# Performance work log

Measured on AMD Instinct MI355X. Metric: run time of the kernel, lower is better.

The kernel has to match this reference:

```python
import jax, jax.numpy as jnp
import numpy as np
from jax import lax

HARD_RANK = 5
HARD_PROB = 0.5
MARGIN = 0.0
EPS = 1e-6  # F.pairwise_distance default eps (added to the difference)


def setup_inputs() -> dict:
    key = jax.random.key(0)
    x = jax.random.normal(key, (8192, 2, 256), dtype=jnp.float32)
    return {"x": x}


def _l2norm(v):
    # torch F.normalize: v / max(||v||, 1e-12)
    n = jnp.sqrt(jnp.sum(v * v, axis=1, keepdims=True))
    return v / jnp.maximum(n, 1e-12)


def reference(x):
    B, _, D = x.shape
    a = _l2norm(x[:, 0, :])  # anchors, unit norm -> ||a_i||^2 = 1
    p = _l2norm(x[:, 1, :])  # positives, unit norm

    # Full anchor-vs-positive distance matrix via GEMM (no [B,B,D] tensor).
    # torch pairwise_distance uses ||a - p + eps||, expand exactly:
    # ||a-p+eps*1||^2 = ||a||^2 + ||p||^2 - 2 a.p + 2*eps*(sum(a)-sum(p)) + D*eps^2
    am = lax.stop_gradient(a)
    pm = lax.stop_gradient(p)
    ip = am @ pm.T                          # [B, B]
    ra = jnp.sum(am, axis=1)                # [B]
    rp = jnp.sum(pm, axis=1)                # [B]
    d2 = 2.0 - 2.0 * ip + 2.0 * EPS * (ra[:, None] - rp[None, :]) + D * EPS * EPS
    dist = jnp.sqrt(jnp.maximum(d2, 0.0))

    # Exclude self (excidx drops idx) by masking diagonal to +inf.
    dmine = jnp.where(jnp.eye(B, dtype=bool), jnp.inf, dist)

    # hard_rank smallest distances per row (rank 0 = hardest negative).
    _, top_idx = lax.top_k(-dmine, HARD_RANK)   # [B, HARD_RANK]

    # With prob hard_prob pick the hardest; else uniform among top hard_rank.
    kr = jax.random.key(1)
    k1, k2 = jax.random.split(kr)
    coin = jax.random.uniform(k1, (B,)) < HARD_PROB
    rand_rank = jax.random.randint(k2, (B,), 0, HARD_RANK)
    rank = jnp.where(coin, 0, rand_rank)
    negidx = top_idx[jnp.arange(B), rank]       # [B]

    neg = p[negidx, :]
    pos_d2 = jnp.sum(jnp.square(a - p + EPS), axis=1)
    neg_d2 = jnp.sum(jnp.square(a - neg + EPS), axis=1)
    return jnp.mean(jax.nn.relu(pos_d2 - neg_d2 + MARGIN))
```

## Files before the change

kernel.cpp:

```cpp
#include <hip/hip_runtime.h>
#include <hip/hip_bf16.h>
#include <stdint.h>


#define NB 8192
#define NCG 32
#define EPSF 1e-6f

typedef int i32x4 __attribute__((ext_vector_type(4)));

struct U2 { uint32_t x, y; };

__host__ __device__ __forceinline__ uint32_t rotl32(uint32_t v, int n) {
  return (v << n) | (v >> (32 - n));
}

__host__ __device__ __forceinline__ U2 tf2x32(uint32_t k0, uint32_t k1,
                                              uint32_t x0, uint32_t x1) {
  uint32_t k2 = k0 ^ k1 ^ 0x1BD11BDAu;
#define TF_R(r) { x0 += x1; x1 = rotl32(x1, r); x1 ^= x0; }
  x0 += k0; x1 += k1;
  TF_R(13) TF_R(15) TF_R(26) TF_R(6)
  x0 += k1; x1 += k2 + 1u;
  TF_R(17) TF_R(29) TF_R(16) TF_R(24)
  x0 += k2; x1 += k0 + 2u;
  TF_R(13) TF_R(15) TF_R(26) TF_R(6)
  x0 += k0; x1 += k1 + 3u;
  TF_R(17) TF_R(29) TF_R(16) TF_R(24)
  x0 += k1; x1 += k2 + 4u;
  TF_R(13) TF_R(15) TF_R(26) TF_R(6)
  x0 += k2; x1 += k0 + 5u;
#undef TF_R
  U2 r; r.x = x0; r.y = x1; return r;
}

__device__ __forceinline__ uint32_t rng_word(U2 r) { return r.x ^ r.y; }

#define FINS5(T0, T1, T2, T3, T4, C) {            \
    const float _t0 = T0, _t1 = T1, _t2 = T2, _t3 = T3, _t4 = T4, _c = C; \
    T0 = fmaxf(_t0, _c);                          \
    T1 = __builtin_amdgcn_fmed3f(_c, _t0, _t1);   \
    T2 = __builtin_amdgcn_fmed3f(_c, _t1, _t2);   \
    T3 = __builtin_amdgcn_fmed3f(_c, _t2, _t3);   \
    T4 = __builtin_amdgcn_fmed3f(_c, _t3, _t4); }

__device__ __forceinline__ void gload16(const void* g, void* l) {
  __builtin_amdgcn_global_load_lds(
      (const __attribute__((address_space(1))) unsigned int*)g,
      (__attribute__((address_space(3))) unsigned int*)l, 16, 0, 0);
}

__global__ __launch_bounds__(256) void prep_kernel(
    const float* __restrict__ x,
    char* __restrict__ aq8, char* __restrict__ pq8) {
  const int w = threadIdx.x >> 6, l = threadIdx.x & 63;
  const int row = blockIdx.x * 4 + w;
  const float4* xr = (const float4*)(x + (size_t)row * 512);
  const float4 a4 = xr[l];
  const float4 p4 = xr[64 + l];
  float sa = a4.x * a4.x + a4.y * a4.y + a4.z * a4.z + a4.w * a4.w;
  float sp = p4.x * p4.x + p4.y * p4.y + p4.z * p4.z + p4.w * p4.w;
#pragma unroll
  for (int off = 32; off; off >>= 1) { sa += __shfl_xor(sa, off); sp += __shfl_xor(sp, off); }
  const float ia = 127.0f / fmaxf(sqrtf(sa), 1e-12f);
  const float ip_ = 127.0f / fmaxf(sqrtf(sp), 1e-12f);
  const int qa0 = (int)rintf(a4.x * ia), qa1 = (int)rintf(a4.y * ia);
  const int qa2 = (int)rintf(a4.z * ia), qa3 = (int)rintf(a4.w * ia);
  const int qp0 = (int)rintf(p4.x * ip_), qp1 = (int)rintf(p4.y * ip_);
  const int qp2 = (int)rintf(p4.z * ip_), qp3 = (int)rintf(p4.w * ip_);
  const uint32_t ua = (qa0 & 255) | ((qa1 & 255) << 8) |
                      ((qa2 & 255) << 16) | ((uint32_t)(qa3 & 255) << 24);
  const uint32_t up = (qp0 & 255) | ((qp1 & 255) << 8) |
                      ((qp2 & 255) << 16) | ((uint32_t)(qp3 & 255) << 24);
  *(uint32_t*)(aq8 + (size_t)row * 256 + l * 4) = ua;
  *(uint32_t*)(pq8 + (size_t)row * 256 + l * 4) = up;
}

__global__ __launch_bounds__(512, 2) void dist_topk_kernel(
    const char* __restrict__ aq8, const char* __restrict__ pq8,
    uint32_t* __restrict__ part) {
  __shared__ __align__(16) char smem[49152];

  const int tid = threadIdx.x;
  const int w = tid >> 6, l = tid & 63;
  const int lo = l & 15, hi = l >> 4;
  const int wr = w >> 2, wc = w & 3;

  const int b = blockIdx.x;
  const int xcd = b & 7, j = b >> 3;
  const int rb = (xcd >> 1) * 16 + (j >> 4);
  const int cb = (xcd & 1) * 16 + (j & 15);
  const int row0 = rb * 128, col0 = cb * 256;
  const bool hasDiag = (cb == (rb >> 1));

  i32x4 acc[4][4];
#pragma unroll
  for (int aq = 0; aq < 4; ++aq)
#pragma unroll
    for (int pq = 0; pq < 4; ++pq) { i32x4 z = {0, 0, 0, 0}; acc[aq][pq] = z; }

#define STAGE(BUF, KS)                                                        \
  {                                                                           \
    { const int off = tid * 16;                                               \
      const int R = off >> 7;                                                 \
      const int s = ((off >> 4) & 7) ^ (R & 7);                               \
      const int r = 2 * R + (s >> 2);                                         \
      const int kb = (s & 3) * 16;                                            \
      gload16(aq8 + (size_t)(row0 + r) * 256 + (KS) * 64 + kb,                \
              smem + (BUF) * 24576 + off); }                                  \
    _Pragma("unroll")                                                         \
    for (int jj = 0; jj < 2; ++jj) {                                          \
      const int off = jj * 8192 + tid * 16;                                   \
      const int R = off >> 7;                                                 \
      const int s = ((off >> 4) & 7) ^ (R & 7);                               \
      const int c = 2 * R + (s >> 2);                                         \
      const int kb = (s & 3) * 16;                                            \
      gload16(pq8 + (size_t)(col0 + c) * 256 + (KS) * 64 + kb,                \
              smem + (BUF) * 24576 + 8192 + off); }                           \
  }

#define LADDR(RR, T) (((RR) >> 1) * 128 + (((((RR) & 1) * 4 + (T)) ^ (((RR) >> 1) & 7)) * 16))

#define COMPUTE(BUF)                                                          \
  {                                                                           \
    i32x4 aF0, aF1, aF2, aF3, bF0, bF1, bF2, bF3;                             \
    { const int r = wr * 64 + 0 + lo;                                         \
      aF0 = __builtin_bit_cast(i32x4, *(const uint4*)(smem + (BUF) * 24576 + LADDR(r, hi))); } \
    { const int r = wr * 64 + 16 + lo;                                        \
      aF1 = __builtin_bit_cast(i32x4, *(const uint4*)(smem + (BUF) * 24576 + LADDR(r, hi))); } \
    { const int r = wr * 64 + 32 + lo;                                        \
      aF2 = __builtin_bit_cast(i32x4, *(const uint4*)(smem + (BUF) * 24576 + LADDR(r, hi))); } \
    { const int r = wr * 64 + 48 + lo;                                        \
      aF3 = __builtin_bit_cast(i32x4, *(const uint4*)(smem + (BUF) * 24576 + LADDR(r, hi))); } \
    { const int c = wc * 64 + 0 + lo;                                         \
      bF0 = __builtin_bit_cast(i32x4, *(const uint4*)(smem + (BUF) * 24576 + 8192 + LADDR(c, hi))); } \
    { const int c = wc * 64 + 16 + lo;                                        \
      bF1 = __builtin_bit_cast(i32x4, *(const uint4*)(smem + (BUF) * 24576 + 8192 + LADDR(c, hi))); } \
    __builtin_amdgcn_s_setprio(1);                                            \
    acc[0][0] = __builtin_amdgcn_mfma_i32_16x16x64_i8(bF0, aF0, acc[0][0], 0, 0, 0); \
    acc[1][0] = __builtin_amdgcn_mfma_i32_16x16x64_i8(bF0, aF1, acc[1][0], 0, 0, 0); \
    acc[2][0] = __builtin_amdgcn_mfma_i32_16x16x64_i8(bF0, aF2, acc[2][0], 0, 0, 0); \
    acc[3][0] = __builtin_amdgcn_mfma_i32_16x16x64_i8(bF0, aF3, acc[3][0], 0, 0, 0); \
    { const int c = wc * 64 + 32 + lo;                                        \
      bF2 = __builtin_bit_cast(i32x4, *(const uint4*)(smem + (BUF) * 24576 + 8192 + LADDR(c, hi))); } \
    acc[0][1] = __builtin_amdgcn_mfma_i32_16x16x64_i8(bF1, aF0, acc[0][1], 0, 0, 0); \
    acc[1][1] = __builtin_amdgcn_mfma_i32_16x16x64_i8(bF1, aF1, acc[1][1], 0, 0, 0); \
    acc[2][1] = __builtin_amdgcn_mfma_i32_16x16x64_i8(bF1, aF2, acc[2][1], 0, 0, 0); \
    acc[3][1] = __builtin_amdgcn_mfma_i32_16x16x64_i8(bF1, aF3, acc[3][1], 0, 0, 0); \
    { const int c = wc * 64 + 48 + lo;                                        \
      bF3 = __builtin_bit_cast(i32x4, *(const uint4*)(smem + (BUF) * 24576 + 8192 + LADDR(c, hi))); } \
    acc[0][2] = __builtin_amdgcn_mfma_i32_16x16x64_i8(bF2, aF0, acc[0][2], 0, 0, 0); \
    acc[1][2] = __builtin_amdgcn_mfma_i32_16x16x64_i8(bF2, aF1, acc[1][2], 0, 0, 0); \
    acc[2][2] = __builtin_amdgcn_mfma_i32_16x16x64_i8(bF2, aF2, acc[2][2], 0, 0, 0); \
    acc[3][2] = __builtin_amdgcn_mfma_i32_16x16x64_i8(bF2, aF3, acc[3][2], 0, 0, 0); \
    acc[0][3] = __builtin_amdgcn_mfma_i32_16x16x64_i8(bF3, aF0, acc[0][3], 0, 0, 0); \
    acc[1][3] = __builtin_amdgcn_mfma_i32_16x16x64_i8(bF3, aF1, acc[1][3], 0, 0, 0); \
    acc[2][3] = __builtin_amdgcn_mfma_i32_16x16x64_i8(bF3, aF2, acc[2][3], 0, 0, 0); \
    acc[3][3] = __builtin_amdgcn_mfma_i32_16x16x64_i8(bF3, aF3, acc[3][3], 0, 0, 0); \
    __builtin_amdgcn_s_setprio(0);                                            \
  }

#define WAITV3 { asm volatile("s_waitcnt vmcnt(3)" ::: "memory"); }
#define WAITV0 { asm volatile("s_waitcnt vmcnt(0)" ::: "memory"); }
#define BAR    { __builtin_amdgcn_s_barrier(); }

  STAGE(0, 0)
  STAGE(1, 1) WAITV3 BAR COMPUTE(0) BAR
  STAGE(0, 2) WAITV3 BAR COMPUTE(1) BAR
  STAGE(1, 3) WAITV3 BAR COMPUTE(0) BAR
  WAITV0 BAR COMPUTE(1)

#undef STAGE
#undef LADDR
#undef COMPUTE
#undef WAITV3
#undef WAITV0
#undef BAR

  __syncthreads();
  uint32_t* mls = (uint32_t*)smem;
  const uint32_t vbase = 8191u - (uint32_t)(col0 + wc * 64) - (uint32_t)(hi * 4);
  const float SC = 1.0f / 16129.0f;
#pragma unroll
  for (int aq = 0; aq < 4; ++aq) {
    float T0 = 0.f, T1 = 0.f, T2 = 0.f, T3 = 0.f, T4 = 0.f;
    const int arow = row0 + wr * 64 + aq * 16 + lo;
#pragma unroll
    for (int pq = 0; pq < 4; ++pq)
#pragma unroll
      for (int r = 0; r < 4; ++r) {
        const float f = fmaf((float)acc[aq][pq][r], SC, 2.0f);
        uint32_t key = (__float_as_uint(f) & 0xFFFFE000u) |
                       (vbase - (uint32_t)(pq * 16 + r));
        if (hasDiag) {
          if (col0 + wc * 64 + pq * 16 + hi * 4 + r == arow) key = 0u;
        }
        const float c = __uint_as_float(key);
        FINS5(T0, T1, T2, T3, T4, c);
      }
    uint32_t* dst = mls + (wr * 64 + aq * 16 + lo) * 81 + (wc * 4 + hi) * 5;
    dst[0] = __float_as_uint(T0);
    dst[1] = __float_as_uint(T1);
    dst[2] = __float_as_uint(T2);
    dst[3] = __float_as_uint(T3);
    dst[4] = __float_as_uint(T4);
  }
  __syncthreads();

  if (tid < 256) {
    const int row = tid >> 1, half = tid & 1;
    const uint32_t* s2 = mls + row * 81 + half * 40;
    float M0 = 0.f, M1 = 0.f, M2 = 0.f, M3 = 0.f, M4 = 0.f;
#pragma unroll
    for (int k = 0; k < 40; ++k) {
      const float c = __uint_as_float(s2[k]);
      FINS5(M0, M1, M2, M3, M4, c);
    }
    const float c0 = __shfl_xor(M0, 1), c1 = __shfl_xor(M1, 1),
                c2 = __shfl_xor(M2, 1), c3 = __shfl_xor(M3, 1),
                c4 = __shfl_xor(M4, 1);
    FINS5(M0, M1, M2, M3, M4, c0);
    FINS5(M0, M1, M2, M3, M4, c1);
    FINS5(M0, M1, M2, M3, M4, c2);
    FINS5(M0, M1, M2, M3, M4, c3);
    FINS5(M0, M1, M2, M3, M4, c4);
    if (half == 0) {
      uint32_t* dst = part + ((size_t)(row0 + row) * NCG + cb) * 5;
      dst[0] = __float_as_uint(M0);
      dst[1] = __float_as_uint(M1);
      dst[2] = __float_as_uint(M2);
      dst[3] = __float_as_uint(M3);
      dst[4] = __float_as_uint(M4);
    }
  }
}

__global__ __launch_bounds__(256) void merge_loss_kernel(
    const float* __restrict__ x, const uint32_t* __restrict__ part,
    float* __restrict__ rowloss,
    uint32_t k1a, uint32_t k1b, uint32_t k2a, uint32_t k2b) {
  const int w = threadIdx.x >> 6, l = threadIdx.x & 63;
  const int i = blockIdx.x * 4 + w;
  __shared__ uint32_t cs[4][160];
  const uint32_t* src = part + (size_t)i * (NCG * 5);
  cs[w][l] = src[l];
  cs[w][64 + l] = src[64 + l];
  if (l < 32) cs[w][128 + l] = src[128 + l];
  __syncthreads();

  float T0 = 0.f, T1 = 0.f, T2 = 0.f, T3 = 0.f, T4 = 0.f;
  for (int rch = 0; rch < NCG; ++rch) {
    for (int q = 0; q < 5; ++q) {
      const float c = __uint_as_float(cs[w][rch * 5 + q]);
      if (c <= T4) break;
      FINS5(T0, T1, T2, T3, T4, c);
    }
  }

  const uint32_t cw = rng_word(tf2x32(k1a, k1b, 0u, (uint32_t)i));
  const bool coin = (cw >> 31) == 0u;
  const uint32_t hb = rng_word(tf2x32(k2a, k2b, 0u, (uint32_t)i));
  const uint32_t lb = rng_word(tf2x32(k2a, k2b, 0u, (uint32_t)(NB + i)));
  const int rr = (int)(((hb % 5u) + (lb % 5u)) % 5u);
  const int rank = coin ? 0 : rr;
  const float kch = (rank == 0) ? T0 : (rank == 1) ? T1 : (rank == 2) ? T2
                  : (rank == 3) ? T3 : T4;
  const int neg = 8191 - (int)(__float_as_uint(kch) & 8191u);

  const float4 xa = *(const float4*)(x + (size_t)i * 512 + l * 4);
  const float4 xp = *(const float4*)(x + (size_t)i * 512 + 256 + l * 4);
  const float4 xn = *(const float4*)(x + (size_t)neg * 512 + 256 + l * 4);
  float sa = xa.x * xa.x + xa.y * xa.y + xa.z * xa.z + xa.w * xa.w;
  float sp = xp.x * xp.x + xp.y * xp.y + xp.z * xp.z + xp.w * xp.w;
  float sn = xn.x * xn.x + xn.y * xn.y + xn.z * xn.z + xn.w * xn.w;
#pragma unroll
  for (int off = 32; off; off >>= 1) {
    sa += __shfl_xor(sa, off); sp += __shfl_xor(sp, off); sn += __shfl_xor(sn, off);
  }
  const float na = fmaxf(sqrtf(sa), 1e-12f);
  const float np = fmaxf(sqrtf(sp), 1e-12f);
  const float nn = fmaxf(sqrtf(sn), 1e-12f);

  float pos = 0.f, ng = 0.f;
  {
    float av, pv, nv, dp, dn;
    av = xa.x / na; pv = xp.x / np; nv = xn.x / nn;
    dp = av - pv + EPSF; pos += dp * dp; dn = av - nv + EPSF; ng += dn * dn;
    av = xa.y / na; pv = xp.y / np; nv = xn.y / nn;
    dp = av - pv + EPSF; pos += dp * dp; dn = av - nv + EPSF; ng += dn * dn;
    av = xa.z / na; pv = xp.z / np; nv = xn.z / nn;
    dp = av - pv + EPSF; pos += dp * dp; dn = av - nv + EPSF; ng += dn * dn;
    av = xa.w / na; pv = xp.w / np; nv = xn.w / nn;
    dp = av - pv + EPSF; pos += dp * dp; dn = av - nv + EPSF; ng += dn * dn;
  }
#pragma unroll
  for (int off = 32; off; off >>= 1) {
    pos += __shfl_xor(pos, off); ng += __shfl_xor(ng, off);
  }
  if (l == 0) rowloss[i] = fmaxf(pos - ng, 0.0f);
}

__global__ __launch_bounds__(256) void finalize_kernel(
    const float* __restrict__ rowloss, float* __restrict__ out) {
  __shared__ float s[256];
  const int t = threadIdx.x;
  float a = 0.f;
  for (int k = 0; k < NB / 256; ++k) a += rowloss[t + 256 * k];
  s[t] = a;
  __syncthreads();
  for (int h = 128; h; h >>= 1) {
    if (t < h) s[t] += s[t + h];
    __syncthreads();
  }
  if (t == 0) out[0] = s[0] / (float)NB;
}

extern "C" void kernel_launch(void* const* d_in, const int* in_sizes, int n_in,
                              void* d_out, int out_size, void* d_ws, size_t ws_size,
                              hipStream_t stream) {
  (void)in_sizes; (void)n_in; (void)out_size; (void)ws_size;
  const float* x = (const float*)d_in[0];
  float* out = (float*)d_out;
  char* ws = (char*)d_ws;

  char* aq8 = ws;
  char* pq8 = ws + (size_t)2 * 1024 * 1024;
  uint32_t* part = (uint32_t*)(ws + (size_t)4 * 1024 * 1024);
  float* rowloss = (float*)(ws + (size_t)4 * 1024 * 1024 +
                            (size_t)NB * NCG * 5 * sizeof(uint32_t));

  U2 c0 = tf2x32(0u, 1u, 0u, 0u);
  U2 c1 = tf2x32(0u, 1u, 0u, 1u);
  const uint32_t k1a = c0.x, k1b = c0.y;
  const uint32_t k2a = c1.x, k2b = c1.y;

  prep_kernel<<<NB / 4, 256, 0, stream>>>(x, aq8, pq8);
  dist_topk_kernel<<<2048, 512, 0, stream>>>(aq8, pq8, part);
  merge_loss_kernel<<<NB / 4, 256, 0, stream>>>(x, part, rowloss, k1a, k1b, k2a, k2b);
  finalize_kernel<<<1, 256, 0, stream>>>(rowloss, out);
}
```

Baseline: 63.76 us.

## Persist A tile across four column blocks and use integer top-5 keys

Each block now keeps its 128-row int8 anchor tile resident in LDS and loops over four 256-column positive tiles. Loading of the next tile's B slice is pipelined behind the current compute, and the grid shrinks from 2048 to 512 blocks. The top-5 selection switches from float-bit keys with fmed3 to integer keys built straight from the int32 dot product, with the column index packed into the low 13 bits. Candidates are reduced with cross-lane shuffles before the LDS merge. The change aims to cut redundant A-tile loads and conversion work, at the cost of more LDS per block (lower occupancy), fewer blocks, and serialized per-tile mining.

```diff
diff --git a/kernel.cpp b/kernel.cpp
--- a/kernel.cpp
+++ b/kernel.cpp
@@ -6,6 +6,7 @@
 #define NB 8192
 #define NCG 32
 #define EPSF 1e-6f
+#define IMIN (-2147483647 - 1)
 
 typedef int i32x4 __attribute__((ext_vector_type(4)));
 
@@ -36,13 +37,13 @@
 
 __device__ __forceinline__ uint32_t rng_word(U2 r) { return r.x ^ r.y; }
 
-#define FINS5(T0, T1, T2, T3, T4, C) {            \
-    const float _t0 = T0, _t1 = T1, _t2 = T2, _t3 = T3, _t4 = T4, _c = C; \
-    T0 = fmaxf(_t0, _c);                          \
-    T1 = __builtin_amdgcn_fmed3f(_c, _t0, _t1);   \
-    T2 = __builtin_amdgcn_fmed3f(_c, _t1, _t2);   \
-    T3 = __builtin_amdgcn_fmed3f(_c, _t2, _t3);   \
-    T4 = __builtin_amdgcn_fmed3f(_c, _t3, _t4); }
+#define FINS5I(T0, T1, T2, T3, T4, C) {           \
+    const int _t0 = T0, _t1 = T1, _t2 = T2, _t3 = T3, _t4 = T4, _c = C; \
+    T0 = _t0 > _c ? _t0 : _c;                     \
+    { const int m = _c < _t0 ? _c : _t0; T1 = _t1 > m ? _t1 : m; } \
+    { const int m = _c < _t1 ? _c : _t1; T2 = _t2 > m ? _t2 : m; } \
+    { const int m = _c < _t2 ? _c : _t2; T3 = _t3 > m ? _t3 : m; } \
+    { const int m = _c < _t3 ? _c : _t3; T4 = _t4 > m ? _t4 : m; } }
 
 __device__ __forceinline__ void gload16(const void* g, void* l) {
   __builtin_amdgcn_global_load_lds(
@@ -79,7 +80,7 @@
 __global__ __launch_bounds__(512, 2) void dist_topk_kernel(
     const char* __restrict__ aq8, const char* __restrict__ pq8,
     uint32_t* __restrict__ part) {
-  __shared__ __align__(16) char smem[49152];
+  __shared__ __align__(16) char smem[76288];
 
   const int tid = threadIdx.x;
   const int w = tid >> 6, l = tid & 63;
@@ -87,27 +88,29 @@
   const int wr = w >> 2, wc = w & 3;
 
   const int b = blockIdx.x;
-  const int xcd = b & 7, j = b >> 3;
-  const int rb = (xcd >> 1) * 16 + (j >> 4);
-  const int cb = (xcd & 1) * 16 + (j & 15);
-  const int row0 = rb * 128, col0 = cb * 256;
-  const bool hasDiag = (cb == (rb >> 1));
+  const int xcd = b & 7, q = b >> 3;
+  const int rb = xcd * 8 + (q & 7);
+  const int cbg = q >> 3;
+  const int row0 = rb * 128;
 
   i32x4 acc[4][4];
-#pragma unroll
-  for (int aq = 0; aq < 4; ++aq)
-#pragma unroll
-    for (int pq = 0; pq < 4; ++pq) { i32x4 z = {0, 0, 0, 0}; acc[aq][pq] = z; }
-
-#define STAGE(BUF, KS)                                                        \
+
+#define STAGE_A                                                               \
   {                                                                           \
-    { const int off = tid * 16;                                               \
+    _Pragma("unroll")                                                         \
+    for (int jj = 0; jj < 4; ++jj) {                                          \
+      const int off = tid * 16;                                               \
       const int R = off >> 7;                                                 \
       const int s = ((off >> 4) & 7) ^ (R & 7);                               \
       const int r = 2 * R + (s >> 2);                                         \
       const int kb = (s & 3) * 16;                                            \
-      gload16(aq8 + (size_t)(row0 + r) * 256 + (KS) * 64 + kb,                \
-              smem + (BUF) * 24576 + off); }                                  \
+      gload16(aq8 + (size_t)(row0 + r) * 256 + jj * 64 + kb,                  \
+              smem + jj * 8192 + off);                                        \
+    }                                                                         \
+  }
+
+#define STAGE_B(BUF, COL0, KS)                                                \
+  {                                                                           \
     _Pragma("unroll")                                                         \
     for (int jj = 0; jj < 2; ++jj) {                                          \
       const int off = jj * 8192 + tid * 16;                                   \
@@ -115,124 +118,134 @@
       const int s = ((off >> 4) & 7) ^ (R & 7);                               \
       const int c = 2 * R + (s >> 2);                                         \
       const int kb = (s & 3) * 16;                                            \
-      gload16(pq8 + (size_t)(col0 + c) * 256 + (KS) * 64 + kb,                \
-              smem + (BUF) * 24576 + 8192 + off); }                           \
-  }
-
-#define LADDR(RR, T) (((RR) >> 1) * 128 + (((((RR) & 1) * 4 + (T)) ^ (((RR) >> 1) & 7)) * 16))
-
-#define COMPUTE(BUF)                                                          \
+      gload16(pq8 + (size_t)((COL0) + c) * 256 + (KS) * 64 + kb,              \
+              smem + 32768 + (BUF) * 16384 + off);                            \
+    }                                                                         \
+  }
+
+#define LADDR(RR, TT) (((RR) >> 1) * 128 + (((((RR) & 1) * 4 + (TT)) ^ (((RR) >> 1) & 7)) * 16))
+
+#define COMPUTE(BUF, KS, Z)                                                   \
   {                                                                           \
     i32x4 aF0, aF1, aF2, aF3, bF0, bF1, bF2, bF3;                             \
     { const int r = wr * 64 + 0 + lo;                                         \
-      aF0 = __builtin_bit_cast(i32x4, *(const uint4*)(smem + (BUF) * 24576 + LADDR(r, hi))); } \
+      aF0 = __builtin_bit_cast(i32x4, *(const uint4*)(smem + (KS) * 8192 + LADDR(r, hi))); } \
     { const int r = wr * 64 + 16 + lo;                                        \
-      aF1 = __builtin_bit_cast(i32x4, *(const uint4*)(smem + (BUF) * 24576 + LADDR(r, hi))); } \
+      aF1 = __builtin_bit_cast(i32x4, *(const uint4*)(smem + (KS) * 8192 + LADDR(r, hi))); } \
     { const int r = wr * 64 + 32 + lo;                                        \
-      aF2 = __builtin_bit_cast(i32x4, *(const uint4*)(smem + (BUF) * 24576 + LADDR(r, hi))); } \
+      aF2 = __builtin_bit_cast(i32x4, *(const uint4*)(smem + (KS) * 8192 + LADDR(r, hi))); } \
     { const int r = wr * 64 + 48 + lo;                                        \
-      aF3 = __builtin_bit_cast(i32x4, *(const uint4*)(smem + (BUF) * 24576 + LADDR(r, hi))); } \
+      aF3 = __builtin_bit_cast(i32x4, *(const uint4*)(smem + (KS) * 8192 + LADDR(r, hi))); } \
     { const int c = wc * 64 + 0 + lo;                                         \
-      bF0 = __builtin_bit_cast(i32x4, *(const uint4*)(smem + (BUF) * 24576 + 8192 + LADDR(c, hi))); } \
+      bF0 = __builtin_bit_cast(i32x4, *(const uint4*)(smem + 32768 + (BUF) * 16384 + LADDR(c, hi))); } \
     { const int c = wc * 64 + 16 + lo;                                        \
-      bF1 = __builtin_bit_cast(i32x4, *(const uint4*)(smem + (BUF) * 24576 + 8192 + LADDR(c, hi))); } \
+      bF1 = __builtin_bit_cast(i32x4, *(const uint4*)(smem + 32768 + (BUF) * 16384 + LADDR(c, hi))); } \
+    i32x4 z = {0, 0, 0, 0};                                                   \
     __builtin_amdgcn_s_setprio(1);                                            \
-    acc[0][0] = __builtin_amdgcn_mfma_i32_16x16x64_i8(bF0, aF0, acc[0][0], 0, 0, 0); \
-    acc[1][0] = __builtin_amdgcn_mfma_i32_16x16x64_i8(bF0, aF1, acc[1][0], 0, 0, 0); \
-    acc[2][0] = __builtin_amdgcn_mfma_i32_16x16x64_i8(bF0, aF2, acc[2][0], 0, 0, 0); \
-    acc[3][0] = __builtin_amdgcn_mfma_i32_16x16x64_i8(bF0, aF3, acc[3][0], 0, 0, 0); \
+    acc[0][0] = __builtin_amdgcn_mfma_i32_16x16x64_i8(bF0, aF0, (Z) ? z : acc[0][0], 0, 0, 0); \
+    acc[1][0] = __builtin_amdgcn_mfma_i32_16x16x64_i8(bF0, aF1, (Z) ? z : acc[1][0], 0, 0, 0); \
+    acc[2][0] = __builtin_amdgcn_mfma_i32_16x16x64_i8(bF0, aF2, (Z) ? z : acc[2][0], 0, 0, 0); \
+    acc[3][0] = __builtin_amdgcn_mfma_i32_16x16x64_i8(bF0, aF3, (Z) ? z : acc[3][0], 0, 0, 0); \
     { const int c = wc * 64 + 32 + lo;                                        \
-      bF2 = __builtin_bit_cast(i32x4, *(const uint4*)(smem + (BUF) * 24576 + 8192 + LADDR(c, hi))); } \
-    acc[0][1] = __builtin_amdgcn_mfma_i32_16x16x64_i8(bF1, aF0, acc[0][1], 0, 0, 0); \
-    acc[1][1] = __builtin_amdgcn_mfma_i32_16x16x64_i8(bF1, aF1, acc[1][1], 0, 0, 0); \
-    acc[2][1] = __builtin_amdgcn_mfma_i32_16x16x64_i8(bF1, aF2, acc[2][1], 0, 0, 0); \
-    acc[3][1] = __builtin_amdgcn_mfma_i32_16x16x64_i8(bF1, aF3, acc[3][1], 0, 0, 0); \
+      bF2 = __builtin_bit_cast(i32x4, *(const uint4*)(smem + 32768 + (BUF) * 16384 + LADDR(c, hi))); } \
+    acc[0][1] = __builtin_amdgcn_mfma_i32_16x16x64_i8(bF1, aF0, (Z) ? z : acc[0][1], 0, 0, 0); \
+    acc[1][1] = __builtin_amdgcn_mfma_i32_16x16x64_i8(bF1, aF1, (Z) ? z : acc[1][1], 0, 0, 0); \
+    acc[2][1] = __builtin_amdgcn_mfma_i32_16x16x64_i8(bF1, aF2, (Z) ? z : acc[2][1], 0, 0, 0); \
+    acc[3][1] = __builtin_amdgcn_mfma_i32_16x16x64_i8(bF1, aF3, (Z) ? z : acc[3][1], 0, 0, 0); \
     { const int c = wc * 64 + 48 + lo;                                        \
-      bF3 = __builtin_bit_cast(i32x4, *(const uint4*)(smem + (BUF) * 24576 + 8192 + LADDR(c, hi))); } \
-    acc[0][2] = __builtin_amdgcn_mfma_i32_16x16x64_i8(bF2, aF0, acc[0][2], 0, 0, 0); \
-    acc[1][2] = __builtin_amdgcn_mfma_i32_16x16x64_i8(bF2, aF1, acc[1][2], 0, 0, 0); \
-    acc[2][2] = __builtin_amdgcn_mfma_i32_16x16x64_i8(bF2, aF2, acc[2][2], 0, 0, 0); \
-    acc[3][2] = __builtin_amdgcn_mfma_i32_16x16x64_i8(bF2, aF3, acc[3][2], 0, 0, 0); \
-    acc[0][3] = __builtin_amdgcn_mfma_i32_16x16x64_i8(bF3, aF0, acc[0][3], 0, 0, 0); \
-    acc[1][3] = __builtin_amdgcn_mfma_i32_16x16x64_i8(bF3, aF1, acc[1][3], 0, 0, 0); \
-    acc[2][3] = __builtin_amdgcn_mfma_i32_16x16x64_i8(bF3, aF2, acc[2][3], 0, 0, 0); \
-    acc[3][3] = __builtin_amdgcn_mfma_i32_16x16x64_i8(bF3, aF3, acc[3][3], 0, 0, 0); \
+      bF3 = __builtin_bit_cast(i32x4, *(const uint4*)(smem + 32768 + (BUF) * 16384 + LADDR(c, hi))); } \
+    acc[0][2] = __builtin_amdgcn_mfma_i32_16x16x64_i8(bF2, aF0, (Z) ? z : acc[0][2], 0, 0, 0); \
+    acc[1][2] = __builtin_amdgcn_mfma_i32_16x16x64_i8(bF2, aF1, (Z) ? z : acc[1][2], 0, 0, 0); \
+    acc[2][2] = __builtin_amdgcn_mfma_i32_16x16x64_i8(bF2, aF2, (Z) ? z : acc[2][2], 0, 0, 0); \
+    acc[3][2] = __builtin_amdgcn_mfma_i32_16x16x64_i8(bF2, aF3, (Z) ? z : acc[3][2], 0, 0, 0); \
+    acc[0][3] = __builtin_amdgcn_mfma_i32_16x16x64_i8(bF3, aF0, (Z) ? z : acc[0][3], 0, 0, 0); \
+    acc[1][3] = __builtin_amdgcn_mfma_i32_16x16x64_i8(bF3, aF1, (Z) ? z : acc[1][3], 0, 0, 0); \
+    acc[2][3] = __builtin_amdgcn_mfma_i32_16x16x64_i8(bF3, aF2, (Z) ? z : acc[2][3], 0, 0, 0); \
+    acc[3][3] = __builtin_amdgcn_mfma_i32_16x16x64_i8(bF3, aF3, (Z) ? z : acc[3][3], 0, 0, 0); \
     __builtin_amdgcn_s_setprio(0);                                            \
   }
 
-#define WAITV3 { asm volatile("s_waitcnt vmcnt(3)" ::: "memory"); }
+#define WAITV2 { asm volatile("s_waitcnt vmcnt(2)" ::: "memory"); }
 #define WAITV0 { asm volatile("s_waitcnt vmcnt(0)" ::: "memory"); }
 #define BAR    { __builtin_amdgcn_s_barrier(); }
 
-  STAGE(0, 0)
-  STAGE(1, 1) WAITV3 BAR COMPUTE(0) BAR
-  STAGE(0, 2) WAITV3 BAR COMPUTE(1) BAR
-  STAGE(1, 3) WAITV3 BAR COMPUTE(0) BAR
-  WAITV0 BAR COMPUTE(1)
-
-#undef STAGE
+#define MINE(COL0)                                                            \
+  {                                                                           \
+    int* mls = (int*)(smem + 65536);                                          \
+    const int cbi = (COL0) >> 8;                                              \
+    const bool hasDiag = (cbi == (rb >> 1));                                  \
+    const int vb13 = 8191 - (COL0) - wc * 64 - hi * 4;                        \
+    _Pragma("unroll")                                                         \
+    for (int aq = 0; aq < 4; ++aq) {                                          \
+      int T0 = IMIN, T1 = IMIN, T2 = IMIN, T3 = IMIN, T4 = IMIN;              \
+      const int arow = row0 + wr * 64 + aq * 16 + lo;                         \
+      _Pragma("unroll")                                                       \
+      for (int pq = 0; pq < 4; ++pq)                                          \
+        _Pragma("unroll")                                                     \
+        for (int rr = 0; rr < 4; ++rr) {                                      \
+          int key = (int)(((uint32_t)acc[aq][pq][rr]) << 13) +                \
+                    (vb13 - (pq * 16 + rr));                                  \
+          if (hasDiag) {                                                      \
+            if ((COL0) + wc * 64 + pq * 16 + hi * 4 + rr == arow) key = IMIN; \
+          }                                                                   \
+          FINS5I(T0, T1, T2, T3, T4, key);                                    \
+        }                                                                     \
+      _Pragma("unroll")                                                       \
+      for (int rd = 0; rd < 2; ++rd) {                                        \
+        const int d = 16 << rd;                                               \
+        const int c0 = __shfl_xor(T0, d), c1 = __shfl_xor(T1, d),             \
+                  c2 = __shfl_xor(T2, d), c3 = __shfl_xor(T3, d),             \
+                  c4 = __shfl_xor(T4, d);                                     \
+        FINS5I(T0, T1, T2, T3, T4, c0);                                       \
+        FINS5I(T0, T1, T2, T3, T4, c1);                                       \
+        FINS5I(T0, T1, T2, T3, T4, c2);                                       \
+        FINS5I(T0, T1, T2, T3, T4, c3);                                       \
+        FINS5I(T0, T1, T2, T3, T4, c4);                                       \
+      }                                                                       \
+      if (hi == 0) {                                                          \
+        int* dst = mls + (wr * 64 + aq * 16 + lo) * 21 + wc * 5;              \
+        dst[0] = T0; dst[1] = T1; dst[2] = T2; dst[3] = T3; dst[4] = T4;      \
+      }                                                                       \
+    }                                                                         \
+    __syncthreads();                                                          \
+    if (tid < 128) {                                                          \
+      const int* s2 = mls + tid * 21;                                         \
+      int M0 = IMIN, M1 = IMIN, M2 = IMIN, M3 = IMIN, M4 = IMIN;              \
+      _Pragma("unroll")                                                       \
+      for (int k = 0; k < 20; ++k) FINS5I(M0, M1, M2, M3, M4, s2[k]);         \
+      int* dst = (int*)part + ((size_t)(row0 + tid) * NCG + cbi) * 5;         \
+      dst[0] = M0; dst[1] = M1; dst[2] = M2; dst[3] = M3; dst[4] = M4;        \
+    }                                                                         \
+  }
+
+  {
+    const int col0 = (cbg * 4 + 0) * 256;
+    STAGE_A
+    STAGE_B(0, col0, 0)
+  }
+#pragma unroll 1
+  for (int t = 0; t < 4; ++t) {
+    const int col0 = (cbg * 4 + t) * 256;
+    STAGE_B(1, col0, 1) WAITV2 BAR COMPUTE(0, 0, 1) BAR
+    STAGE_B(0, col0, 2) WAITV2 BAR COMPUTE(1, 1, 0) BAR
+    STAGE_B(1, col0, 3) WAITV2 BAR COMPUTE(0, 2, 0) BAR
+    if (t < 3) {
+      const int col0n = col0 + 256;
+      STAGE_B(0, col0n, 0) WAITV2 BAR COMPUTE(1, 3, 0) BAR
+    } else {
+      WAITV0 BAR COMPUTE(1, 3, 0)
+    }
+    MINE(col0)
+  }
+
+#undef STAGE_A
+#undef STAGE_B
 #undef LADDR
 #undef COMPUTE
-#undef WAITV3
+#undef WAITV2
 #undef WAITV0
 #undef BAR
-
-  __syncthreads();
-  uint32_t* mls = (uint32_t*)smem;
-  const uint32_t vbase = 8191u - (uint32_t)(col0 + wc * 64) - (uint32_t)(hi * 4);
-  const float SC = 1.0f / 16129.0f;
-#pragma unroll
-  for (int aq = 0; aq < 4; ++aq) {
-    float T0 = 0.f, T1 = 0.f, T2 = 0.f, T3 = 0.f, T4 = 0.f;
-    const int arow = row0 + wr * 64 + aq * 16 + lo;
-#pragma unroll
-    for (int pq = 0; pq < 4; ++pq)
-#pragma unroll
-      for (int r = 0; r < 4; ++r) {
-        const float f = fmaf((float)acc[aq][pq][r], SC, 2.0f);
-        uint32_t key = (__float_as_uint(f) & 0xFFFFE000u) |
-                       (vbase - (uint32_t)(pq * 16 + r));
-        if (hasDiag) {
-          if (col0 + wc * 64 + pq * 16 + hi * 4 + r == arow) key = 0u;
-        }
-        const float c = __uint_as_float(key);
-        FINS5(T0, T1, T2, T3, T4, c);
-      }
-    uint32_t* dst = mls + (wr * 64 + aq * 16 + lo) * 81 + (wc * 4 + hi) * 5;
-    dst[0] = __float_as_uint(T0);
-    dst[1] = __float_as_uint(T1);
-    dst[2] = __float_as_uint(T2);
-    dst[3] = __float_as_uint(T3);
-    dst[4] = __float_as_uint(T4);
-  }
-  __syncthreads();
-
-  if (tid < 256) {
-    const int row = tid >> 1, half = tid & 1;
-    const uint32_t* s2 = mls + row * 81 + half * 40;
-    float M0 = 0.f, M1 = 0.f, M2 = 0.f, M3 = 0.f, M4 = 0.f;
-#pragma unroll
-    for (int k = 0; k < 40; ++k) {
-      const float c = __uint_as_float(s2[k]);
-      FINS5(M0, M1, M2, M3, M4, c);
-    }
-    const float c0 = __shfl_xor(M0, 1), c1 = __shfl_xor(M1, 1),
-                c2 = __shfl_xor(M2, 1), c3 = __shfl_xor(M3, 1),
-                c4 = __shfl_xor(M4, 1);
-    FINS5(M0, M1, M2, M3, M4, c0);
-    FINS5(M0, M1, M2, M3, M4, c1);
-    FINS5(M0, M1, M2, M3, M4, c2);
-    FINS5(M0, M1, M2, M3, M4, c3);
-    FINS5(M0, M1, M2, M3, M4, c4);
-    if (half == 0) {
-      uint32_t* dst = part + ((size_t)(row0 + row) * NCG + cb) * 5;
-      dst[0] = __float_as_uint(M0);
-      dst[1] = __float_as_uint(M1);
-      dst[2] = __float_as_uint(M2);
-      dst[3] = __float_as_uint(M3);
-      dst[4] = __float_as_uint(M4);
-    }
-  }
+#undef MINE
 }
 
 __global__ __launch_bounds__(256) void merge_loss_kernel(
@@ -241,19 +254,19 @@
     uint32_t k1a, uint32_t k1b, uint32_t k2a, uint32_t k2b) {
   const int w = threadIdx.x >> 6, l = threadIdx.x & 63;
   const int i = blockIdx.x * 4 + w;
-  __shared__ uint32_t cs[4][160];
-  const uint32_t* src = part + (size_t)i * (NCG * 5);
+  __shared__ int cs[4][160];
+  const int* src = (const int*)part + (size_t)i * (NCG * 5);
   cs[w][l] = src[l];
   cs[w][64 + l] = src[64 + l];
   if (l < 32) cs[w][128 + l] = src[128 + l];
   __syncthreads();
 
-  float T0 = 0.f, T1 = 0.f, T2 = 0.f, T3 = 0.f, T4 = 0.f;
+  int T0 = IMIN, T1 = IMIN, T2 = IMIN, T3 = IMIN, T4 = IMIN;
   for (int rch = 0; rch < NCG; ++rch) {
     for (int q = 0; q < 5; ++q) {
-      const float c = __uint_as_float(cs[w][rch * 5 + q]);
+      const int c = cs[w][rch * 5 + q];
       if (c <= T4) break;
-      FINS5(T0, T1, T2, T3, T4, c);
+      FINS5I(T0, T1, T2, T3, T4, c);
     }
   }
 
@@ -263,9 +276,9 @@
   const uint32_t lb = rng_word(tf2x32(k2a, k2b, 0u, (uint32_t)(NB + i)));
   const int rr = (int)(((hb % 5u) + (lb % 5u)) % 5u);
   const int rank = coin ? 0 : rr;
-  const float kch = (rank == 0) ? T0 : (rank == 1) ? T1 : (rank == 2) ? T2
-                  : (rank == 3) ? T3 : T4;
-  const int neg = 8191 - (int)(__float_as_uint(kch) & 8191u);
+  const int kch = (rank == 0) ? T0 : (rank == 1) ? T1 : (rank == 2) ? T2
+                : (rank == 3) ? T3 : T4;
+  const int neg = 8191 - (kch & 8191);
 
   const float4 xa = *(const float4*)(x + (size_t)i * 512 + l * 4);
   const float4 xp = *(const float4*)(x + (size_t)i * 512 + 256 + l * 4);
@@ -335,7 +348,7 @@
   const uint32_t k2a = c1.x, k2b = c1.y;
 
   prep_kernel<<<NB / 4, 256, 0, stream>>>(x, aq8, pq8);
-  dist_topk_kernel<<<2048, 512, 0, stream>>>(aq8, pq8, part);
+  dist_topk_kernel<<<512, 512, 0, stream>>>(aq8, pq8, part);
   merge_loss_kernel<<<NB / 4, 256, 0, stream>>>(x, part, rowloss, k1a, k1b, k2a, k2b);
   finalize_kernel<<<1, 256, 0, stream>>>(rowloss, out);
 }
```

New measurement: 83.16 us. +30.4%, slower.

## Use integer top-k keys and fuse final reduction via atomics

Applied to the files above, without the earlier changes.

Builds top-5 selection keys directly from the int32 MFMA accumulators shifted left and combined with the column index, using integer med3, instead of converting to float per element. The separate finalize kernel is removed: merge_loss accumulates row losses as fixed-point 64-bit atomics, and the last block, found through a counter, writes the mean. This saves conversion ALU work and one kernel launch, at the cost of a memset and possible overflow of the shifted key range.

```diff
diff --git a/kernel.cpp b/kernel.cpp
--- a/kernel.cpp
+++ b/kernel.cpp
@@ -6,6 +6,7 @@
 #define NB 8192
 #define NCG 32
 #define EPSF 1e-6f
+#define IMIN (-2147483647 - 1)
 
 typedef int i32x4 __attribute__((ext_vector_type(4)));
 
@@ -36,13 +37,13 @@
 
 __device__ __forceinline__ uint32_t rng_word(U2 r) { return r.x ^ r.y; }
 
-#define FINS5(T0, T1, T2, T3, T4, C) {            \
-    const float _t0 = T0, _t1 = T1, _t2 = T2, _t3 = T3, _t4 = T4, _c = C; \
-    T0 = fmaxf(_t0, _c);                          \
-    T1 = __builtin_amdgcn_fmed3f(_c, _t0, _t1);   \
-    T2 = __builtin_amdgcn_fmed3f(_c, _t1, _t2);   \
-    T3 = __builtin_amdgcn_fmed3f(_c, _t2, _t3);   \
-    T4 = __builtin_amdgcn_fmed3f(_c, _t3, _t4); }
+#define FINS5I(T0, T1, T2, T3, T4, C) {           \
+    const int _c = (C), _t0 = T0, _t1 = T1, _t2 = T2, _t3 = T3, _t4 = T4; \
+    T0 = _t0 > _c ? _t0 : _c;                     \
+    asm("v_med3_i32 %0, %1, %2, %3" : "=v"(T1) : "v"(_c), "v"(_t0), "v"(_t1)); \
+    asm("v_med3_i32 %0, %1, %2, %3" : "=v"(T2) : "v"(_c), "v"(_t1), "v"(_t2)); \
+    asm("v_med3_i32 %0, %1, %2, %3" : "=v"(T3) : "v"(_c), "v"(_t2), "v"(_t3)); \
+    asm("v_med3_i32 %0, %1, %2, %3" : "=v"(T4) : "v"(_c), "v"(_t3), "v"(_t4)); }
 
 __device__ __forceinline__ void gload16(const void* g, void* l) {
   __builtin_amdgcn_global_load_lds(
@@ -78,7 +79,7 @@
 
 __global__ __launch_bounds__(512, 2) void dist_topk_kernel(
     const char* __restrict__ aq8, const char* __restrict__ pq8,
-    uint32_t* __restrict__ part) {
+    int* __restrict__ part) {
   __shared__ __align__(16) char smem[49152];
 
   const int tid = threadIdx.x;
@@ -178,82 +179,69 @@
 #undef BAR
 
   __syncthreads();
-  uint32_t* mls = (uint32_t*)smem;
-  const uint32_t vbase = 8191u - (uint32_t)(col0 + wc * 64) - (uint32_t)(hi * 4);
-  const float SC = 1.0f / 16129.0f;
+  int* mls = (int*)smem;
+  const int vb13 = 8191 - (col0 + wc * 64) - hi * 4;
 #pragma unroll
   for (int aq = 0; aq < 4; ++aq) {
-    float T0 = 0.f, T1 = 0.f, T2 = 0.f, T3 = 0.f, T4 = 0.f;
+    int T0 = IMIN, T1 = IMIN, T2 = IMIN, T3 = IMIN, T4 = IMIN;
     const int arow = row0 + wr * 64 + aq * 16 + lo;
 #pragma unroll
     for (int pq = 0; pq < 4; ++pq)
 #pragma unroll
-      for (int r = 0; r < 4; ++r) {
-        const float f = fmaf((float)acc[aq][pq][r], SC, 2.0f);
-        uint32_t key = (__float_as_uint(f) & 0xFFFFE000u) |
-                       (vbase - (uint32_t)(pq * 16 + r));
+      for (int rr = 0; rr < 4; ++rr) {
+        int key = (int)(((uint32_t)acc[aq][pq][rr]) << 13) + vb13 - (pq * 16 + rr);
         if (hasDiag) {
-          if (col0 + wc * 64 + pq * 16 + hi * 4 + r == arow) key = 0u;
+          if (col0 + wc * 64 + pq * 16 + hi * 4 + rr == arow) key = IMIN;
         }
-        const float c = __uint_as_float(key);
-        FINS5(T0, T1, T2, T3, T4, c);
+        FINS5I(T0, T1, T2, T3, T4, key);
       }
-    uint32_t* dst = mls + (wr * 64 + aq * 16 + lo) * 81 + (wc * 4 + hi) * 5;
-    dst[0] = __float_as_uint(T0);
-    dst[1] = __float_as_uint(T1);
-    dst[2] = __float_as_uint(T2);
-    dst[3] = __float_as_uint(T3);
-    dst[4] = __float_as_uint(T4);
+    int* dst = mls + (wr * 64 + aq * 16 + lo) * 81 + (wc * 4 + hi) * 5;
+    dst[0] = T0; dst[1] = T1; dst[2] = T2; dst[3] = T3; dst[4] = T4;
   }
   __syncthreads();
 
   if (tid < 256) {
     const int row = tid >> 1, half = tid & 1;
-    const uint32_t* s2 = mls + row * 81 + half * 40;
-    float M0 = 0.f, M1 = 0.f, M2 = 0.f, M3 = 0.f, M4 = 0.f;
-#pragma unroll
-    for (int k = 0; k < 40; ++k) {
-      const float c = __uint_as_float(s2[k]);
-      FINS5(M0, M1, M2, M3, M4, c);
+    const int* s2 = mls + row * 81 + half * 40;
+    int M0 = IMIN, M1 = IMIN, M2 = IMIN, M3 = IMIN, M4 = IMIN;
+#pragma unroll
+    for (int k = 0; k < 40; ++k) FINS5I(M0, M1, M2, M3, M4, s2[k]);
+    const int c0 = __shfl_xor(M0, 1), c1 = __shfl_xor(M1, 1),
+              c2 = __shfl_xor(M2, 1), c3 = __shfl_xor(M3, 1),
+              c4 = __shfl_xor(M4, 1);
+    FINS5I(M0, M1, M2, M3, M4, c0);
+    FINS5I(M0, M1, M2, M3, M4, c1);
+    FINS5I(M0, M1, M2, M3, M4, c2);
+    FINS5I(M0, M1, M2, M3, M4, c3);
+    FINS5I(M0, M1, M2, M3, M4, c4);
+    if (half == 0) {
+      int* dst = part + ((size_t)(row0 + row) * NCG + cb) * 5;
+      dst[0] = M0; dst[1] = M1; dst[2] = M2; dst[3] = M3; dst[4] = M4;
     }
-    const float c0 = __shfl_xor(M0, 1), c1 = __shfl_xor(M1, 1),
-                c2 = __shfl_xor(M2, 1), c3 = __shfl_xor(M3, 1),
-                c4 = __shfl_xor(M4, 1);
-    FINS5(M0, M1, M2, M3, M4, c0);
-    FINS5(M0, M1, M2, M3, M4, c1);
-    FINS5(M0, M1, M2, M3, M4, c2);
-    FINS5(M0, M1, M2, M3, M4, c3);
-    FINS5(M0, M1, M2, M3, M4, c4);
-    if (half == 0) {
-      uint32_t* dst = part + ((size_t)(row0 + row) * NCG + cb) * 5;
-      dst[0] = __float_as_uint(M0);
-      dst[1] = __float_as_uint(M1);
-      dst[2] = __float_as_uint(M2);
-      dst[3] = __float_as_uint(M3);
-      dst[4] = __float_as_uint(M4);
-    }
   }
 }
 
 __global__ __launch_bounds__(256) void merge_loss_kernel(
-    const float* __restrict__ x, const uint32_t* __restrict__ part,
-    float* __restrict__ rowloss,
+    const float* __restrict__ x, const int* __restrict__ part,
+    unsigned long long* __restrict__ acc64, unsigned int* __restrict__ cnt,
+    float* __restrict__ out,
     uint32_t k1a, uint32_t k1b, uint32_t k2a, uint32_t k2b) {
   const int w = threadIdx.x >> 6, l = threadIdx.x & 63;
   const int i = blockIdx.x * 4 + w;
-  __shared__ uint32_t cs[4][160];
-  const uint32_t* src = part + (size_t)i * (NCG * 5);
+  __shared__ int cs[4][160];
+  __shared__ unsigned long long bsum[4];
+  const int* src = part + (size_t)i * (NCG * 5);
   cs[w][l] = src[l];
   cs[w][64 + l] = src[64 + l];
   if (l < 32) cs[w][128 + l] = src[128 + l];
   __syncthreads();
 
-  float T0 = 0.f, T1 = 0.f, T2 = 0.f, T3 = 0.f, T4 = 0.f;
+  int T0 = IMIN, T1 = IMIN, T2 = IMIN, T3 = IMIN, T4 = IMIN;
   for (int rch = 0; rch < NCG; ++rch) {
     for (int q = 0; q < 5; ++q) {
-      const float c = __uint_as_float(cs[w][rch * 5 + q]);
+      const int c = cs[w][rch * 5 + q];
       if (c <= T4) break;
-      FINS5(T0, T1, T2, T3, T4, c);
+      FINS5I(T0, T1, T2, T3, T4, c);
     }
   }
 
@@ -263,9 +251,9 @@
   const uint32_t lb = rng_word(tf2x32(k2a, k2b, 0u, (uint32_t)(NB + i)));
   const int rr = (int)(((hb % 5u) + (lb % 5u)) % 5u);
   const int rank = coin ? 0 : rr;
-  const float kch = (rank == 0) ? T0 : (rank == 1) ? T1 : (rank == 2) ? T2
-                  : (rank == 3) ? T3 : T4;
-  const int neg = 8191 - (int)(__float_as_uint(kch) & 8191u);
+  const int kch = (rank == 0) ? T0 : (rank == 1) ? T1 : (rank == 2) ? T2
+                : (rank == 3) ? T3 : T4;
+  const int neg = 8191 - (kch & 8191);
 
   const float4 xa = *(const float4*)(x + (size_t)i * 512 + l * 4);
   const float4 xp = *(const float4*)(x + (size_t)i * 512 + 256 + l * 4);
@@ -297,22 +285,22 @@
   for (int off = 32; off; off >>= 1) {
     pos += __shfl_xor(pos, off); ng += __shfl_xor(ng, off);
   }
-  if (l == 0) rowloss[i] = fmaxf(pos - ng, 0.0f);
-}
-
-__global__ __launch_bounds__(256) void finalize_kernel(
-    const float* __restrict__ rowloss, float* __restrict__ out) {
-  __shared__ float s[256];
-  const int t = threadIdx.x;
-  float a = 0.f;
-  for (int k = 0; k < NB / 256; ++k) a += rowloss[t + 256 * k];
-  s[t] = a;
+  if (l == 0) {
+    const float rl = fmaxf(pos - ng, 0.0f);
+    bsum[w] = (unsigned long long)((double)rl * 4294967296.0);
+  }
   __syncthreads();
-  for (int h = 128; h; h >>= 1) {
-    if (t < h) s[t] += s[t + h];
-    __syncthreads();
-  }
-  if (t == 0) out[0] = s[0] / (float)NB;
+
+  if (threadIdx.x == 0) {
+    const unsigned long long s4 = bsum[0] + bsum[1] + bsum[2] + bsum[3];
+    atomicAdd(acc64, s4);
+    __threadfence();
+    const unsigned int old = atomicAdd(cnt, 1u);
+    if (old == gridDim.x - 1) {
+      const unsigned long long total = atomicAdd(acc64, 0ULL);
+      out[0] = (float)((double)total / 4294967296.0 / (double)NB);
+    }
+  }
 }
 
 extern "C" void kernel_launch(void* const* d_in, const int* in_sizes, int n_in,
@@ -325,17 +313,20 @@
 
   char* aq8 = ws;
   char* pq8 = ws + (size_t)2 * 1024 * 1024;
-  uint32_t* part = (uint32_t*)(ws + (size_t)4 * 1024 * 1024);
-  float* rowloss = (float*)(ws + (size_t)4 * 1024 * 1024 +
-                            (size_t)NB * NCG * 5 * sizeof(uint32_t));
+  int* part = (int*)(ws + (size_t)4 * 1024 * 1024);
+  char* tail = ws + (size_t)4 * 1024 * 1024 +
+               (size_t)NB * NCG * 5 * sizeof(int);
+  unsigned long long* acc64 = (unsigned long long*)tail;
+  unsigned int* cnt = (unsigned int*)(tail + 8);
 
   U2 c0 = tf2x32(0u, 1u, 0u, 0u);
   U2 c1 = tf2x32(0u, 1u, 0u, 1u);
   const uint32_t k1a = c0.x, k1b = c0.y;
   const uint32_t k2a = c1.x, k2b = c1.y;
 
+  hipMemsetAsync(tail, 0, 16, stream);
   prep_kernel<<<NB / 4, 256, 0, stream>>>(x, aq8, pq8);
   dist_topk_kernel<<<2048, 512, 0, stream>>>(aq8, pq8, part);
-  merge_loss_kernel<<<NB / 4, 256, 0, stream>>>(x, part, rowloss, k1a, k1b, k2a, k2b);
-  finalize_kernel<<<1, 256, 0, stream>>>(rowloss, out);
-}
+  merge_loss_kernel<<<NB / 4, 256, 0, stream>>>(x, part, acc64, cnt, out,
+                                                k1a, k1b, k2a, k2b);
+}
```

Measured after the change: 109.0 us. 1.71x slower.
